# Kernel tuning notes

Hardware: AMD Instinct MI355X
Metric: run time of the kernel (lower is better)

Reference implementation:

```python
import jax, jax.numpy as jnp
import numpy as np

K = 20
EPS = 1e-5
SLOPE = 0.2


def _knn_idx(x, k):
    # x: [B, C, N] -> idx [B, N, k] of nearest neighbors by squared L2
    sq = jnp.sum(x * x, axis=1)                      # [B, N]
    inner = jnp.einsum('bcn,bcm->bnm', x, x)         # [B, N, N]
    neg_dist = 2.0 * inner - sq[:, :, None] - sq[:, None, :]
    return jax.lax.top_k(neg_dist, k)[1]             # [B, N, k]


def _edge_block(x, W, gamma, beta, k):
    # x: [B, C, N]; W: [O, 2C]; returns [B, O, N]
    idx = _knn_idx(x, k)
    xt = jnp.transpose(x, (0, 2, 1))                 # [B, N, C]
    nb = jax.vmap(lambda t, i: t[i])(xt, idx)        # [B, N, k, C] gather
    ctr = xt[:, :, None, :]
    edge = jnp.concatenate(
        [nb - ctr, jnp.broadcast_to(ctr, nb.shape)], axis=-1)  # [B, N, k, 2C]
    y = jnp.einsum('bnkc,oc->bonk', edge, W)         # 1x1 conv
    # BatchNorm2d (training mode: batch stats over B,N,k per channel)
    m = jnp.mean(y, axis=(0, 2, 3), keepdims=True)
    v = jnp.var(y, axis=(0, 2, 3), keepdims=True)
    y = (y - m) * jax.lax.rsqrt(v + EPS)
    y = y * gamma[None, :, None, None] + beta[None, :, None, None]
    y = jnp.where(y >= 0, y, SLOPE * y)              # LeakyReLU(0.2)
    return jnp.max(y, axis=-1)                       # max over k neighbors


def setup_inputs() -> dict:
    key = jax.random.key(0)
    ks = jax.random.split(key, 8)
    B, N = 8, 2048
    x = jax.random.normal(ks[0], (B, N, 3), dtype=jnp.float32)
    W1 = jax.random.normal(ks[1], (64, 6), dtype=jnp.float32) * 0.2
    W2 = jax.random.normal(ks[2], (128, 128), dtype=jnp.float32) * 0.08
    W3 = jax.random.normal(ks[3], (256, 256), dtype=jnp.float32) * 0.06
    g1, b1 = jnp.ones((64,), jnp.float32), jnp.zeros((64,), jnp.float32)
    g2, b2 = jnp.ones((128,), jnp.float32), jnp.zeros((128,), jnp.float32)
    g3, b3 = jnp.ones((256,), jnp.float32), jnp.zeros((256,), jnp.float32)
    L1 = jax.random.normal(ks[4], (1024, 448), dtype=jnp.float32) * 0.04
    L2 = jax.random.normal(ks[5], (2500, 1024), dtype=jnp.float32) * 0.03
    return {"x": x, "W1": W1, "g1": g1, "b1": b1, "W2": W2, "g2": g2,
            "b2": b2, "W3": W3, "g3": g3, "b3": b3, "L1": L1, "L2": L2}


def reference(x, W1, g1, b1, W2, g2, b2, W3, g3, b3, L1, L2):
    xT = jnp.transpose(x, (0, 2, 1))                 # [B, 3, N]
    x1 = _edge_block(xT, W1, g1, b1, K)              # [B, 64, N]
    x2 = _edge_block(x1, W2, g2, b2, K)              # [B, 128, N]
    x3 = _edge_block(x2, W3, g3, b3, K)              # [B, 256, N]
    feat = jnp.concatenate([x1, x2, x3], axis=1)     # [B, 448, N]
    pooled = jnp.max(feat, axis=-1)                  # adaptive_max_pool1d(1)
    h = pooled @ L1.T
    h = jnp.where(h >= 0, h, SLOPE * h)              # LeakyReLU(0.2)
    # dropout is identity in eval mode
    return h @ L2.T                                  # [B, 2500]
```

## Files before the change

kernel.cpp:

```cpp
#include <hip/hip_runtime.h>
#include <hip/hip_bf16.h>
#include <float.h>

#define K_NN 20
#define EPS 1e-5f
#define SLOPE 0.2f
constexpr int Bsz = 8;
constexpr int Npts = 2048;
constexpr int NQ = 8;
constexpr int BN = Bsz * Npts;

typedef __attribute__((ext_vector_type(8))) short short8v;
typedef __attribute__((ext_vector_type(4))) float f32x4;

__device__ __forceinline__ float dot4(float4 a, float4 b) {
  return a.x*b.x + a.y*b.y + a.z*b.z + a.w*b.w;
}
__device__ __forceinline__ unsigned encf(float f) {
  unsigned u = __float_as_uint(f);
  return (u & 0x80000000u) ? ~u : (u | 0x80000000u);
}
__device__ __forceinline__ float decf(unsigned e) {
  unsigned u = (e & 0x80000000u) ? (e & 0x7fffffffu) : ~e;
  return __uint_as_float(u);
}
__device__ __forceinline__ unsigned short f2bf(float x) {
  unsigned u = __float_as_uint(x);
  unsigned r = (u + 0x7fffu + ((u >> 16) & 1u)) >> 16;
  return (unsigned short)r;
}
__device__ __forceinline__ float bf2f(unsigned short h) {
  return __uint_as_float((unsigned)h << 16);
}
__device__ __forceinline__ f32x4 mfma16(short8v a, short8v b, f32x4 c) {
  return __builtin_amdgcn_mfma_f32_16x16x32_bf16(a, b, c, 0, 0, 0);
}

template<int C>
__global__ __launch_bounds__(256) void sq_kernel(const float* __restrict__ xt,
                                                 float* __restrict__ sq) {
  int p = blockIdx.x * 256 + threadIdx.x;
  if (p >= BN) return;
  const float* r = xt + (size_t)p * C;
  float s = 0.f;
  if constexpr (C % 4 == 0) {
    for (int c4 = 0; c4 < C / 4; ++c4) { float4 v = *(const float4*)(r + c4 * 4); s += dot4(v, v); }
  } else {
    #pragma unroll
    for (int c = 0; c < C; ++c) { float v = r[c]; s += v * v; }
  }
  sq[p] = s;
}

template<int C, int MT>
__global__ __launch_bounds__(256) void knn_part(const float* __restrict__ xt,
    const float* __restrict__ sq, float* __restrict__ pval, int* __restrict__ pidx) {
  constexpr int MQ = Npts / NQ;
  __shared__ __align__(16) float chk[MT][C];
  __shared__ float csq[MT];
  const int t = threadIdx.x, w = t >> 6, l = t & 63;
  const int rowblk = blockIdx.x / NQ;
  const int q = blockIdx.x - rowblk * NQ;
  const int p0 = rowblk * 256;
  const int b = p0 / Npts;
  const int myrow = p0 + w * 64 + l;

  float cr[C];
  #pragma unroll
  for (int c = 0; c < C; ++c) cr[c] = xt[(size_t)myrow * C + c];
  const float sqn = sq[myrow];

  float vals[K_NN]; int ids[K_NN];
  #pragma unroll
  for (int i = 0; i < K_NN; ++i) { vals[i] = -FLT_MAX; ids[i] = 0; }

  const int mbase = q * MQ;
  for (int m0 = mbase; m0 < mbase + MQ; m0 += MT) {
    __syncthreads();
    const float* s2 = xt + ((size_t)b * Npts + m0) * C;
    for (int e = t; e < MT * C; e += 256) chk[e / C][e - (e / C) * C] = s2[e];
    for (int e = t; e < MT; e += 256) csq[e] = sq[b * Npts + m0 + e];
    __syncthreads();
    for (int j = 0; j < MT; ++j) {
      float dt = 0.f;
      #pragma unroll
      for (int c = 0; c < C; ++c) dt += cr[c] * chk[j][c];
      float nd = 2.f * dt - sqn - csq[j];
      if (nd > vals[K_NN - 1]) {
        vals[K_NN - 1] = nd; ids[K_NN - 1] = m0 + j;
        #pragma unroll
        for (int i = K_NN - 1; i >= 1; --i) {
          if (vals[i] > vals[i - 1]) {
            float tv = vals[i]; vals[i] = vals[i-1]; vals[i-1] = tv;
            int ti = ids[i]; ids[i] = ids[i-1]; ids[i-1] = ti;
          }
        }
      }
    }
  }
  size_t base = ((size_t)q * BN + myrow) * K_NN;
  #pragma unroll
  for (int i = 0; i < K_NN; ++i) { pval[base + i] = vals[i]; pidx[base + i] = ids[i]; }
}

__global__ __launch_bounds__(256) void knn_merge(const float* __restrict__ pval,
    const int* __restrict__ pidx, int* __restrict__ idxout) {
  int p = blockIdx.x * 256 + threadIdx.x;
  if (p >= BN) return;
  float vals[K_NN]; int ids[K_NN];
  size_t base = (size_t)p * K_NN;
  #pragma unroll
  for (int i = 0; i < K_NN; ++i) { vals[i] = pval[base + i]; ids[i] = pidx[base + i]; }
  for (int q = 1; q < NQ; ++q) {
    size_t b2 = ((size_t)q * BN + p) * K_NN;
    #pragma unroll
    for (int i = 0; i < K_NN; ++i) {
      float v = pval[b2 + i];
      if (v <= vals[K_NN - 1]) break;
      int m = pidx[b2 + i];
      vals[K_NN - 1] = v; ids[K_NN - 1] = m;
      #pragma unroll
      for (int r = K_NN - 1; r >= 1; --r) {
        if (vals[r] > vals[r - 1]) {
          float tv = vals[r]; vals[r] = vals[r-1]; vals[r-1] = tv;
          int ti = ids[r]; ids[r] = ids[r-1]; ids[r-1] = ti;
        }
      }
    }
  }
  int* op = idxout + (size_t)p * K_NN;
  #pragma unroll
  for (int i = 0; i < K_NN; ++i) op[i] = ids[i];
}

template<int C>
__global__ __launch_bounds__(64) void knn_fused(
    const unsigned short* __restrict__ xh, const unsigned short* __restrict__ xl,
    const float* __restrict__ sq, int* __restrict__ idxout) {
  constexpr int KS = C / 32;
  const int b = blockIdx.x >> 7, qt = blockIdx.x & 127;
  const int q0 = qt * 16;
  const int l = threadIdx.x, l15 = l & 15, grp = l >> 4;
  const unsigned short* xbh = xh + (size_t)b * Npts * C;
  const unsigned short* xbl = xl + (size_t)b * Npts * C;
  const float* sqb = sq + b * Npts;
  const int qi = q0 + l15;

  short8v bh[KS], bl[KS];
  #pragma unroll
  for (int ks = 0; ks < KS; ++ks) {
    const size_t a = (size_t)qi * C + ks * 32 + grp * 8;
    bh[ks] = *(const short8v*)(xbh + a);
    bl[ks] = *(const short8v*)(xbl + a);
  }
  const float sqn = sqb[qi];

  float vals[K_NN]; int ids[K_NN];
  #pragma unroll
  for (int i = 0; i < K_NN; ++i) { vals[i] = -FLT_MAX; ids[i] = 0; }

  for (int mt = 0; mt < Npts / 64; ++mt) {
    const int m0 = mt * 64;
    f32x4 acc[4];
    #pragma unroll
    for (int rt = 0; rt < 4; ++rt) acc[rt] = (f32x4){0.f, 0.f, 0.f, 0.f};
    #pragma unroll
    for (int ks = 0; ks < KS; ++ks) {
      #pragma unroll
      for (int rt = 0; rt < 4; ++rt) {
        const size_t aoff = (size_t)(m0 + rt * 16 + l15) * C + ks * 32 + grp * 8;
        const short8v a_h = *(const short8v*)(xbh + aoff);
        const short8v a_l = *(const short8v*)(xbl + aoff);
        acc[rt] = mfma16(a_h, bh[ks], acc[rt]);
        acc[rt] = mfma16(a_l, bh[ks], acc[rt]);
        acc[rt] = mfma16(a_h, bl[ks], acc[rt]);
      }
    }
    #pragma unroll
    for (int rt = 0; rt < 4; ++rt) {
      const int cb = m0 + rt * 16 + grp * 4;
      const float4 s4 = *(const float4*)(sqb + cb);
      const float sv[4] = {s4.x, s4.y, s4.z, s4.w};
      #pragma unroll
      for (int r = 0; r < 4; ++r) {
        const int cand = cb + r;
        float v = 2.f * acc[rt][r] - sqn - sv[r];
        if (cand == qi) v = 0.f;
        if (v > vals[K_NN - 1]) {
          vals[K_NN - 1] = v; ids[K_NN - 1] = cand;
          #pragma unroll
          for (int i = K_NN - 1; i >= 1; --i) {
            if (vals[i] > vals[i - 1]) {
              float tv = vals[i]; vals[i] = vals[i-1]; vals[i-1] = tv;
              int ti = ids[i]; ids[i] = ids[i-1]; ids[i-1] = ti;
            }
          }
        }
      }
    }
  }

  #pragma unroll
  for (int s2 = 1; s2 < 4; ++s2) {
    float ov[K_NN]; int oi[K_NN];
    #pragma unroll
    for (int i = 0; i < K_NN; ++i) {
      ov[i] = __shfl(vals[i], s2 * 16 + l15);
      oi[i] = __shfl(ids[i],  s2 * 16 + l15);
    }
    if (grp == 0) {
      #pragma unroll
      for (int i = 0; i < K_NN; ++i) {
        const float v = ov[i];
        if (v <= vals[K_NN - 1]) break;
        vals[K_NN - 1] = v; ids[K_NN - 1] = oi[i];
        #pragma unroll
        for (int r = K_NN - 1; r >= 1; --r) {
          if (vals[r] > vals[r - 1]) {
            float tv = vals[r]; vals[r] = vals[r-1]; vals[r-1] = tv;
            int ti = ids[r]; ids[r] = ids[r-1]; ids[r-1] = ti;
          }
        }
      }
    }
  }
  if (grp == 0) {
    int* op = idxout + ((size_t)(b * Npts + qi)) * K_NN;
    #pragma unroll
    for (int i = 0; i < K_NN; ++i) op[i] = ids[i];
  }
}

template<int C, int O>
__global__ __launch_bounds__(256) void prep_w(const float* __restrict__ W,
    unsigned short* __restrict__ wh, unsigned short* __restrict__ wl) {
  int i = blockIdx.x * 256 + threadIdx.x;
  if (i >= 2 * O * C) return;
  int j = i / C, c = i - j * C;
  float v = (j < O) ? W[(size_t)j * 2 * C + c]
                    : (W[(size_t)(j - O) * 2 * C + C + c] - W[(size_t)(j - O) * 2 * C + c]);
  unsigned short h = f2bf(v);
  wh[i] = h; wl[i] = f2bf(v - bf2f(h));
}

template<int C, int N2>
__global__ __launch_bounds__(256) void zgemm(
    const unsigned short* __restrict__ xh, const unsigned short* __restrict__ xl,
    const unsigned short* __restrict__ wh, const unsigned short* __restrict__ wl,
    float* __restrict__ Z, int r0) {
  constexpr int KS = C / 32;
  constexpr int CB = N2 / 64;
  const int nb = blockIdx.x / CB, cb = blockIdx.x - nb * CB;
  const int ln0 = nb * 64;
  const int t = threadIdx.x, l = t & 63, wv = t >> 6, l15 = l & 15, grp = l >> 4;
  const int col = cb * 64 + wv * 16 + l15;
  f32x4 acc[4];
  #pragma unroll
  for (int rt = 0; rt < 4; ++rt) acc[rt] = (f32x4){0.f, 0.f, 0.f, 0.f};
  #pragma unroll
  for (int ks = 0; ks < KS; ++ks) {
    const int krd = ks * 32 + grp * 8;
    const short8v bh = *(const short8v*)(wh + (size_t)col * C + krd);
    const short8v bl = *(const short8v*)(wl + (size_t)col * C + krd);
    #pragma unroll
    for (int rt = 0; rt < 4; ++rt) {
      const size_t arow = (size_t)(r0 + ln0 + rt * 16 + l15) * C + krd;
      const short8v a_h = *(const short8v*)(xh + arow);
      const short8v a_l = *(const short8v*)(xl + arow);
      acc[rt] = mfma16(a_h, bh, acc[rt]);
      acc[rt] = mfma16(a_l, bh, acc[rt]);
      acc[rt] = mfma16(a_h, bl, acc[rt]);
    }
  }
  #pragma unroll
  for (int rt = 0; rt < 4; ++rt)
    #pragma unroll
    for (int r = 0; r < 4; ++r)
      Z[(size_t)(ln0 + rt * 16 + grp * 4 + r) * N2 + col] = acc[rt][r];
}

template<int O, int NPP>
__global__ __launch_bounds__(256) void nbr_reduce(
    const float* __restrict__ Z, const int* __restrict__ idx,
    float* __restrict__ mx, float* __restrict__ mn,
    float* __restrict__ psum, float* __restrict__ psq, int r0) {
  constexpr int PPB = 256 / O;
  constexpr int O2 = 2 * O;
  const int t = threadIdx.x;
  const int o = t % O;
  const int sub = t / O;
  float ls = 0.f, lq = 0.f;
  for (int it = 0; it < NPP / PPB; ++it) {
    const int p = r0 + blockIdx.x * NPP + it * PPB + sub;
    const int bbase = (p >> 11) << 11;
    const int* ip = idx + (size_t)p * K_NN;
    const float base = Z[(size_t)(p - r0) * O2 + O + o];
    float vmx = -FLT_MAX, vmn = FLT_MAX;
    #pragma unroll
    for (int k = 0; k < K_NN; ++k) {
      const int nbrow = bbase + ip[k] - r0;
      const float y = Z[(size_t)nbrow * O2 + o] + base;
      ls += y; lq = fmaf(y, y, lq);
      vmx = fmaxf(vmx, y); vmn = fminf(vmn, y);
    }
    mx[(size_t)p * O + o] = vmx;
    mn[(size_t)p * O + o] = vmn;
  }
  if constexpr (PPB > 1) {
    __shared__ float s1[256], s2[256];
    s1[t] = ls; s2[t] = lq;
    __syncthreads();
    if (sub == 0) {
      psum[(size_t)blockIdx.x * O + o] = ls + s1[t + O];
      psq [(size_t)blockIdx.x * O + o] = lq + s2[t + O];
    }
  } else {
    psum[(size_t)blockIdx.x * O + o] = ls;
    psq [(size_t)blockIdx.x * O + o] = lq;
  }
}

template<int C, int O, int G, int NPG, int CPT>
__global__ __launch_bounds__(256) void edge_kernel(const float* __restrict__ xt,
    const int* __restrict__ idx, const float* __restrict__ W,
    float* __restrict__ mx, float* __restrict__ mn,
    float* __restrict__ psum, float* __restrict__ psq) {
  constexpr int WP = O / (64 * CPT);
  constexpr int TPB = 64 * WP * NPG;
  constexpr int PPG = G / NPG;
  static_assert(TPB == 256, "block must be 256 threads");
  __shared__ __align__(16) float pts[G][K_NN + 1][C];
  __shared__ int ids[G][K_NN + 1];
  __shared__ float shps[NPG][O];
  __shared__ float shpq[NPG][O];
  const int t = threadIdx.x;
  const int p0 = blockIdx.x * G;
  const int b = p0 / Npts;

  for (int e = t; e < G * (K_NN + 1); e += TPB) {
    int g = e / (K_NN + 1), j = e - g * (K_NN + 1);
    ids[g][j] = (j == 0) ? (p0 + g) : (b * Npts + idx[(size_t)(p0 + g) * K_NN + (j - 1)]);
  }
  __syncthreads();
  for (int e = t; e < G * (K_NN + 1) * C; e += TPB) {
    int g = e / ((K_NN + 1) * C), rem = e - g * ((K_NN + 1) * C);
    int j = rem / C, c = rem - j * C;
    pts[g][j][c] = xt[(size_t)ids[g][j] * C + c];
  }
  __syncthreads();

  const int w = t >> 6, l = t & 63;
  const int pg = w / WP, wp = w - pg * WP;
  const int o0 = wp * 64 + l;
  float ls0 = 0.f, lq0 = 0.f;

  for (int it = 0; it < PPG; ++it) {
    const int g = pg * PPG + it;
    float yk0[K_NN];
    float u0 = 0.f, v0 = 0.f;
    #pragma unroll
    for (int k = 0; k < K_NN; ++k) yk0[k] = 0.f;
    const float* W0 = W + (size_t)o0 * (2 * C);
    #pragma unroll
    for (int c = 0; c < C; ++c) {
      const float wl = W0[c], whv = W0[C + c], ccv = pts[g][0][c];
      u0 += wl * ccv; v0 += whv * ccv;
      #pragma unroll
      for (int k = 0; k < K_NN; ++k) yk0[k] += wl * pts[g][k + 1][c];
    }
    const int n = p0 + g - b * Npts;
    const size_t obase = ((size_t)b * Npts + n) * O;
    const float base = v0 - u0;
    float vmx = -FLT_MAX, vmn = FLT_MAX;
    #pragma unroll
    for (int k = 0; k < K_NN; ++k) {
      float y = yk0[k] + base;
      ls0 += y; lq0 += y * y;
      vmx = fmaxf(vmx, y); vmn = fminf(vmn, y);
    }
    mx[obase + o0] = vmx; mn[obase + o0] = vmn;
  }

  shps[pg][o0] = ls0; shpq[pg][o0] = lq0;
  __syncthreads();
  if (t < O) {
    float s = 0.f, qq = 0.f;
    #pragma unroll
    for (int i = 0; i < NPG; ++i) { s += shps[i][t]; qq += shpq[i][t]; }
    psum[(size_t)blockIdx.x * O + t] = s;
    psq [(size_t)blockIdx.x * O + t] = qq;
  }
}

template<int O, int NBLK>
__global__ __launch_bounds__(256) void stats_part(const float* __restrict__ psum,
    const float* __restrict__ psq, double* __restrict__ pp, double* __restrict__ pq) {
  constexpr int NS = 16;
  constexpr int SL = NBLK / NS;
  const int l = threadIdx.x & 63, w = threadIdx.x >> 6;
  const int os = blockIdx.x % (O / 64), sl = blockIdx.x / (O / 64);
  const int o = os * 64 + l;
  double s = 0.0, ss = 0.0;
  for (int i = sl * SL + w; i < (sl + 1) * SL; i += 4) {
    s  += (double)psum[(size_t)i * O + o];
    ss += (double)psq [(size_t)i * O + o];
  }
  __shared__ double sh[2][4][64];
  sh[0][w][l] = s; sh[1][w][l] = ss;
  __syncthreads();
  if (w == 0) {
    s  = sh[0][0][l] + sh[0][1][l] + sh[0][2][l] + sh[0][3][l];
    ss = sh[1][0][l] + sh[1][1][l] + sh[1][2][l] + sh[1][3][l];
    pp[(size_t)sl * O + o] = s;
    pq[(size_t)sl * O + o] = ss;
  }
}

template<int O>
__global__ __launch_bounds__(64) void stats_final(const double* __restrict__ pp,
    const double* __restrict__ pq,
    const float* __restrict__ gamma, const float* __restrict__ beta,
    float* __restrict__ scale, float* __restrict__ bias) {
  const int o = blockIdx.x * 64 + threadIdx.x;
  double s = 0.0, ss = 0.0;
  #pragma unroll
  for (int sl = 0; sl < 16; ++sl) { s += pp[(size_t)sl * O + o]; ss += pq[(size_t)sl * O + o]; }
  double cnt = (double)Bsz * Npts * K_NN;
  double m = s / cnt;
  double var = ss / cnt - m * m;
  float g = gamma[o];
  float sc = g * rsqrtf((float)var + EPS);
  scale[o] = sc;
  bias[o] = beta[o] - (float)m * sc;
}

__global__ __launch_bounds__(256) void reset_pool(unsigned* __restrict__ pooled) {
  int i = blockIdx.x * 256 + threadIdx.x;
  if (i < Bsz * 448) pooled[i] = 0u;
}

template<int O, int COFF, bool WNC>
__global__ __launch_bounds__(256) void apply_kernel(const float* __restrict__ mx,
    const float* __restrict__ mn, const float* __restrict__ scale,
    const float* __restrict__ bias, float* __restrict__ xnc,
    unsigned short* __restrict__ xh, unsigned short* __restrict__ xl,
    unsigned* __restrict__ pooled) {
  constexpr int OT = O / 64;
  constexpr int NCH = Npts / 256;
  const int bid = blockIdx.x;
  const int nchunk = bid % NCH;
  const int ot = (bid / NCH) % OT;
  const int b = bid / (NCH * OT);
  const int l = threadIdx.x & 63, w = threadIdx.x >> 6;
  const int o = ot * 64 + l;
  const float sc = scale[o], bs = bias[o];
  const bool pos = (sc >= 0.f);
  float vmax = -FLT_MAX;
  const int n0 = nchunk * 256;
  for (int i = 0; i < 64; ++i) {
    int n = n0 + w + i * 4;
    size_t ix = ((size_t)b * Npts + n) * O + o;
    float raw = pos ? mx[ix] : mn[ix];
    float y = raw * sc + bs;
    y = (y >= 0.f) ? y : SLOPE * y;
    if constexpr (WNC) {
      xnc[ix] = y;
      unsigned short h = f2bf(y);
      xh[ix] = h;
      xl[ix] = f2bf(y - bf2f(h));
    }
    vmax = fmaxf(vmax, y);
  }
  __shared__ float sh[4][64];
  sh[w][l] = vmax;
  __syncthreads();
  if (w == 0) {
    float m = fmaxf(fmaxf(sh[0][l], sh[1][l]), fmaxf(sh[2][l], sh[3][l]));
    atomicMax(pooled + b * 448 + COFF + o, encf(m));
  }
}

template<int CIN, bool LRELU, bool DECODE>
__global__ __launch_bounds__(64) void fc_kernel(const void* __restrict__ inv,
    const float* __restrict__ Wt, float* __restrict__ out, int JO) {
  int j = blockIdx.x;
  const float* wr = Wt + (size_t)j * CIN;
  float acc[Bsz];
  #pragma unroll
  for (int b = 0; b < Bsz; ++b) acc[b] = 0.f;
  for (int c = threadIdx.x; c < CIN; c += 64) {
    float wv = wr[c];
    #pragma unroll
    for (int b = 0; b < Bsz; ++b) {
      float x;
      if constexpr (DECODE) x = decf(((const unsigned*)inv)[b * CIN + c]);
      else                  x = ((const float*)inv)[b * CIN + c];
      acc[b] += x * wv;
    }
  }
  #pragma unroll
  for (int b = 0; b < Bsz; ++b) {
    float v = acc[b];
    #pragma unroll
    for (int w = 32; w > 0; w >>= 1) v += __shfl_down(v, w);
    if (threadIdx.x == 0) {
      if (LRELU) v = (v >= 0.f) ? v : SLOPE * v;
      out[b * JO + j] = v;
    }
  }
}

extern "C" void kernel_launch(void* const* d_in, const int* in_sizes, int n_in,
                              void* d_out, int out_size, void* d_ws, size_t ws_size,
                              hipStream_t stream) {
  const float* x   = (const float*)d_in[0];
  const float* W1  = (const float*)d_in[1];
  const float* g1  = (const float*)d_in[2];
  const float* b1  = (const float*)d_in[3];
  const float* W2  = (const float*)d_in[4];
  const float* g2  = (const float*)d_in[5];
  const float* b2  = (const float*)d_in[6];
  const float* W3  = (const float*)d_in[7];
  const float* g3  = (const float*)d_in[8];
  const float* b3  = (const float*)d_in[9];
  const float* L1  = (const float*)d_in[10];
  const float* L2  = (const float*)d_in[11];
  float* out = (float*)d_out;

  float* ws = (float*)d_ws;
  size_t off = 0;
  float* sq    = ws + off; off += BN;
  int*   idxb  = (int*)(ws + off); off += (size_t)BN * K_NN;
  float* mx    = ws + off; off += (size_t)BN * 256;
  float* mn    = ws + off; off += (size_t)BN * 256;
  float* Z     = ws + off; off += (size_t)BN * 256;
  float* psum  = ws + off; off += (size_t)2048 * 256;
  float* psq   = ws + off; off += (size_t)2048 * 256;
  off = (off + 1) & ~(size_t)1;
  double* pp   = (double*)(ws + off); off += 16 * 256 * 2;
  double* pq   = (double*)(ws + off); off += 16 * 256 * 2;
  float* scale = ws + off; off += 256;
  float* bias  = ws + off; off += 256;
  float* x1nc  = ws + off; off += (size_t)BN * 64;
  float* x2nc  = ws + off; off += (size_t)BN * 128;
  unsigned short* xh1 = (unsigned short*)(ws + off); off += (size_t)BN * 64 / 2;
  unsigned short* xl1 = (unsigned short*)(ws + off); off += (size_t)BN * 64 / 2;
  unsigned short* xh2 = (unsigned short*)(ws + off); off += (size_t)BN * 128 / 2;
  unsigned short* xl2 = (unsigned short*)(ws + off); off += (size_t)BN * 128 / 2;
  unsigned* pooled = (unsigned*)(ws + off); off += Bsz * 448;
  float* h     = ws + off; off += Bsz * 1024;
  unsigned short* wch2 = (unsigned short*)(ws + off); off += 256 * 64 / 2;
  unsigned short* wcl2 = (unsigned short*)(ws + off); off += 256 * 64 / 2;
  unsigned short* wch3 = (unsigned short*)(ws + off); off += 512 * 128 / 2;
  unsigned short* wcl3 = (unsigned short*)(ws + off); off += 512 * 128 / 2;
  float* pval = mx;
  int*   pidx = (int*)mn;

  reset_pool<<<14, 256, 0, stream>>>(pooled);
  prep_w<64, 128><<<(2 * 128 * 64 + 255) / 256, 256, 0, stream>>>(W2, wch2, wcl2);
  prep_w<128, 256><<<(2 * 256 * 128 + 255) / 256, 256, 0, stream>>>(W3, wch3, wcl3);

  sq_kernel<3><<<64, 256, 0, stream>>>(x, sq);
  knn_part<3, 64><<<(BN / 256) * NQ, 256, 0, stream>>>(x, sq, pval, pidx);
  knn_merge<<<64, 256, 0, stream>>>(pval, pidx, idxb);
  edge_kernel<3, 64, 16, 4, 1><<<BN / 16, 256, 0, stream>>>(x, idxb, W1, mx, mn, psum, psq);
  stats_part<64, 1024><<<16, 256, 0, stream>>>(psum, psq, pp, pq);
  stats_final<64><<<1, 64, 0, stream>>>(pp, pq, g1, b1, scale, bias);
  apply_kernel<64, 0, true><<<64, 256, 0, stream>>>(mx, mn, scale, bias, x1nc, xh1, xl1, pooled);

  sq_kernel<64><<<64, 256, 0, stream>>>(x1nc, sq);
  knn_fused<64><<<Bsz * 128, 64, 0, stream>>>(xh1, xl1, sq, idxb);
  zgemm<64, 256><<<(BN / 64) * 4, 256, 0, stream>>>(xh1, xl1, wch2, wcl2, Z, 0);
  nbr_reduce<128, 16><<<BN / 16, 256, 0, stream>>>(Z, idxb, mx, mn, psum, psq, 0);
  stats_part<128, 1024><<<32, 256, 0, stream>>>(psum, psq, pp, pq);
  stats_final<128><<<2, 64, 0, stream>>>(pp, pq, g2, b2, scale, bias);
  apply_kernel<128, 64, true><<<128, 256, 0, stream>>>(mx, mn, scale, bias, x2nc, xh2, xl2, pooled);

  sq_kernel<128><<<64, 256, 0, stream>>>(x2nc, sq);
  knn_fused<128><<<Bsz * 128, 64, 0, stream>>>(xh2, xl2, sq, idxb);
  for (int pass = 0; pass < 2; ++pass) {
    const int r0 = pass * (BN / 2);
    zgemm<128, 512><<<(BN / 2 / 64) * 8, 256, 0, stream>>>(xh2, xl2, wch3, wcl3, Z, r0);
    nbr_reduce<256, 8><<<BN / 2 / 8, 256, 0, stream>>>(Z, idxb, mx, mn,
        psum + (size_t)pass * 1024 * 256, psq + (size_t)pass * 1024 * 256, r0);
  }
  stats_part<256, 2048><<<64, 256, 0, stream>>>(psum, psq, pp, pq);
  stats_final<256><<<4, 64, 0, stream>>>(pp, pq, g3, b3, scale, bias);
  apply_kernel<256, 192, false><<<256, 256, 0, stream>>>(mx, mn, scale, bias, nullptr, nullptr, nullptr, pooled);

  fc_kernel<448, true, true><<<1024, 64, 0, stream>>>(pooled, L1, h, 1024);
  fc_kernel<1024, false, false><<<2500, 64, 0, stream>>>(h, L2, out, 2500);
}
```

Measured before the change: 1.238 ms.

## Split knn_fused candidate scan across four waves and merge via LDS; early-exit insertion

knn_fused now launches 256 threads per block, and each of the four wavefronts scans a quarter of the candidate points for the same 16 queries. The per-wave top-K lists are written to shared memory and merged by 16 threads after a barrier. Separately, the insertion-sort bubble loops in all kNN kernels now break as soon as the new element is in place. This is meant to add parallelism for the 1024-block grid and cut wasted compare/swap work, at the cost of an LDS merge, a block sync, and more divergent branches in unrolled loops.

```diff
diff --git a/kernel.cpp b/kernel.cpp
--- a/kernel.cpp
+++ b/kernel.cpp
@@ -93,7 +93,7 @@
           if (vals[i] > vals[i - 1]) {
             float tv = vals[i]; vals[i] = vals[i-1]; vals[i-1] = tv;
             int ti = ids[i]; ids[i] = ids[i-1]; ids[i-1] = ti;
-          }
+          } else break;
         }
       }
     }
@@ -124,7 +124,7 @@
         if (vals[r] > vals[r - 1]) {
           float tv = vals[r]; vals[r] = vals[r-1]; vals[r-1] = tv;
           int ti = ids[r]; ids[r] = ids[r-1]; ids[r-1] = ti;
-        }
+        } else break;
       }
     }
   }
@@ -134,13 +134,16 @@
 }
 
 template<int C>
-__global__ __launch_bounds__(64) void knn_fused(
+__global__ __launch_bounds__(256) void knn_fused(
     const unsigned short* __restrict__ xh, const unsigned short* __restrict__ xl,
     const float* __restrict__ sq, int* __restrict__ idxout) {
   constexpr int KS = C / 32;
+  constexpr int TPW = Npts / 64 / 4;
+  __shared__ float svv[4][16][K_NN];
+  __shared__ int   sii[4][16][K_NN];
   const int b = blockIdx.x >> 7, qt = blockIdx.x & 127;
   const int q0 = qt * 16;
-  const int l = threadIdx.x, l15 = l & 15, grp = l >> 4;
+  const int t = threadIdx.x, wv = t >> 6, l = t & 63, l15 = l & 15, grp = l >> 4;
   const unsigned short* xbh = xh + (size_t)b * Npts * C;
   const unsigned short* xbl = xl + (size_t)b * Npts * C;
   const float* sqb = sq + b * Npts;
@@ -159,7 +162,7 @@
   #pragma unroll
   for (int i = 0; i < K_NN; ++i) { vals[i] = -FLT_MAX; ids[i] = 0; }
 
-  for (int mt = 0; mt < Npts / 64; ++mt) {
+  for (int mt = wv * TPW; mt < (wv + 1) * TPW; ++mt) {
     const int m0 = mt * 64;
     f32x4 acc[4];
     #pragma unroll
@@ -193,7 +196,7 @@
             if (vals[i] > vals[i - 1]) {
               float tv = vals[i]; vals[i] = vals[i-1]; vals[i-1] = tv;
               int ti = ids[i]; ids[i] = ids[i-1]; ids[i-1] = ti;
-            }
+            } else break;
           }
         }
       }
@@ -219,13 +222,34 @@
           if (vals[r] > vals[r - 1]) {
             float tv = vals[r]; vals[r] = vals[r-1]; vals[r-1] = tv;
             int ti = ids[r]; ids[r] = ids[r-1]; ids[r-1] = ti;
-          }
+          } else break;
         }
       }
     }
   }
   if (grp == 0) {
-    int* op = idxout + ((size_t)(b * Npts + qi)) * K_NN;
+    #pragma unroll
+    for (int i = 0; i < K_NN; ++i) { svv[wv][l15][i] = vals[i]; sii[wv][l15][i] = ids[i]; }
+  }
+  __syncthreads();
+  if (t < 16) {
+    #pragma unroll
+    for (int s2 = 1; s2 < 4; ++s2) {
+      #pragma unroll
+      for (int i = 0; i < K_NN; ++i) {
+        const float v = svv[s2][t][i];
+        if (v <= vals[K_NN - 1]) break;
+        vals[K_NN - 1] = v; ids[K_NN - 1] = sii[s2][t][i];
+        #pragma unroll
+        for (int r = K_NN - 1; r >= 1; --r) {
+          if (vals[r] > vals[r - 1]) {
+            float tv = vals[r]; vals[r] = vals[r-1]; vals[r-1] = tv;
+            int ti = ids[r]; ids[r] = ids[r-1]; ids[r-1] = ti;
+          } else break;
+        }
+      }
+    }
+    int* op = idxout + ((size_t)(b * Npts + q0 + t)) * K_NN;
     #pragma unroll
     for (int i = 0; i < K_NN; ++i) op[i] = ids[i];
   }
@@ -569,7 +593,7 @@
   apply_kernel<64, 0, true><<<64, 256, 0, stream>>>(mx, mn, scale, bias, x1nc, xh1, xl1, pooled);
 
   sq_kernel<64><<<64, 256, 0, stream>>>(x1nc, sq);
-  knn_fused<64><<<Bsz * 128, 64, 0, stream>>>(xh1, xl1, sq, idxb);
+  knn_fused<64><<<Bsz * 128, 256, 0, stream>>>(xh1, xl1, sq, idxb);
   zgemm<64, 256><<<(BN / 64) * 4, 256, 0, stream>>>(xh1, xl1, wch2, wcl2, Z, 0);
   nbr_reduce<128, 16><<<BN / 16, 256, 0, stream>>>(Z, idxb, mx, mn, psum, psq, 0);
   stats_part<128, 1024><<<32, 256, 0, stream>>>(psum, psq, pp, pq);
@@ -577,7 +601,7 @@
   apply_kernel<128, 64, true><<<128, 256, 0, stream>>>(mx, mn, scale, bias, x2nc, xh2, xl2, pooled);
 
   sq_kernel<128><<<64, 256, 0, stream>>>(x2nc, sq);
-  knn_fused<128><<<Bsz * 128, 64, 0, stream>>>(xh2, xl2, sq, idxb);
+  knn_fused<128><<<Bsz * 128, 256, 0, stream>>>(xh2, xl2, sq, idxb);
   for (int pass = 0; pass < 2; ++pass) {
     const int r0 = pass * (BN / 2);
     zgemm<128, 512><<<(BN / 2 / 64) * 8, 256, 0, stream>>>(xh2, xl2, wch3, wcl3, Z, r0);
```

After: 3.011 ms. 2.43x slower.

## Replace per-lane insertion-sort top-k with two-pass radix select in shared memory

Applied to the files above, without the earlier changes.

The fused KNN kernel for layers 2 and 3 now uses 256 threads per block of 16 queries. It finds the top-20 by building shared-memory byte histograms over the encoded distance keys, selecting the threshold bucket in two radix passes, then collecting candidates above the threshold and resolving the boundary bucket. This replaces the register insertion sort with branchy swaps per candidate, at the cost of recomputing the distance MFMA three times and contending on shared-memory atomics. A 160-entry cap on the boundary bucket could drop candidates if many keys tie in the top 16 bits. Output indices are sorted by index rather than by distance, and knn_merge gains a template parameter so its merge loop can be unrolled.

```diff
diff --git a/kernel.cpp b/kernel.cpp
--- a/kernel.cpp
+++ b/kernel.cpp
@@ -103,6 +103,7 @@
   for (int i = 0; i < K_NN; ++i) { pval[base + i] = vals[i]; pidx[base + i] = ids[i]; }
 }
 
+template<int NQM>
 __global__ __launch_bounds__(256) void knn_merge(const float* __restrict__ pval,
     const int* __restrict__ pidx, int* __restrict__ idxout) {
   int p = blockIdx.x * 256 + threadIdx.x;
@@ -111,7 +112,8 @@
   size_t base = (size_t)p * K_NN;
   #pragma unroll
   for (int i = 0; i < K_NN; ++i) { vals[i] = pval[base + i]; ids[i] = pidx[base + i]; }
-  for (int q = 1; q < NQ; ++q) {
+  #pragma unroll
+  for (int q = 1; q < NQM; ++q) {
     size_t b2 = ((size_t)q * BN + p) * K_NN;
     #pragma unroll
     for (int i = 0; i < K_NN; ++i) {
@@ -134,13 +136,19 @@
 }
 
 template<int C>
-__global__ __launch_bounds__(64) void knn_fused(
+__global__ __launch_bounds__(256) void knn_radix(
     const unsigned short* __restrict__ xh, const unsigned short* __restrict__ xl,
     const float* __restrict__ sq, int* __restrict__ idxout) {
   constexpr int KS = C / 32;
+  constexpr int CAP = 160;
+  __shared__ unsigned hist[16][257];
+  __shared__ unsigned outb[16][K_NN];
+  __shared__ unsigned bkey[16][CAP];
+  __shared__ unsigned bidx[16][CAP];
+  __shared__ unsigned sb1[16], sneed1[16], sprefix[16], sneed2[16], ocnt[16], bct[16];
   const int b = blockIdx.x >> 7, qt = blockIdx.x & 127;
   const int q0 = qt * 16;
-  const int l = threadIdx.x, l15 = l & 15, grp = l >> 4;
+  const int t = threadIdx.x, wv = t >> 6, l = t & 63, l15 = l & 15, grp = l >> 4;
   const unsigned short* xbh = xh + (size_t)b * Npts * C;
   const unsigned short* xbl = xl + (size_t)b * Npts * C;
   const float* sqb = sq + b * Npts;
@@ -155,12 +163,7 @@
   }
   const float sqn = sqb[qi];
 
-  float vals[K_NN]; int ids[K_NN];
-  #pragma unroll
-  for (int i = 0; i < K_NN; ++i) { vals[i] = -FLT_MAX; ids[i] = 0; }
-
-  for (int mt = 0; mt < Npts / 64; ++mt) {
-    const int m0 = mt * 64;
+  auto compute_keys = [&](int m0, unsigned* keys) {
     f32x4 acc[4];
     #pragma unroll
     for (int rt = 0; rt < 4; ++rt) acc[rt] = (f32x4){0.f, 0.f, 0.f, 0.f};
@@ -183,51 +186,121 @@
       const float sv[4] = {s4.x, s4.y, s4.z, s4.w};
       #pragma unroll
       for (int r = 0; r < 4; ++r) {
-        const int cand = cb + r;
         float v = 2.f * acc[rt][r] - sqn - sv[r];
-        if (cand == qi) v = 0.f;
-        if (v > vals[K_NN - 1]) {
-          vals[K_NN - 1] = v; ids[K_NN - 1] = cand;
-          #pragma unroll
-          for (int i = K_NN - 1; i >= 1; --i) {
-            if (vals[i] > vals[i - 1]) {
-              float tv = vals[i]; vals[i] = vals[i-1]; vals[i-1] = tv;
-              int ti = ids[i]; ids[i] = ids[i-1]; ids[i-1] = ti;
-            }
+        if (cb + r == qi) v = 0.f;
+        keys[rt * 4 + r] = encf(v);
+      }
+    }
+  };
+
+  for (int i = t; i < 16 * 257; i += 256) ((unsigned*)hist)[i] = 0u;
+  __syncthreads();
+  #pragma unroll 1
+  for (int ti = 0; ti < 8; ++ti) {
+    unsigned keys[16];
+    compute_keys((wv * 8 + ti) * 64, keys);
+    #pragma unroll
+    for (int i = 0; i < 16; ++i) atomicAdd(&hist[l15][keys[i] >> 24], 1u);
+  }
+  __syncthreads();
+  if (t < 16) {
+    unsigned cum = 0, na = 0; int b1 = 0, found = 0;
+    for (int bin = 255; bin >= 0; --bin) {
+      unsigned c = hist[t][bin];
+      if (!found && cum + c >= K_NN) { b1 = bin; na = cum; found = 1; }
+      cum += c;
+    }
+    sb1[t] = (unsigned)b1; sneed1[t] = K_NN - na;
+  }
+  __syncthreads();
+  for (int i = t; i < 16 * 257; i += 256) ((unsigned*)hist)[i] = 0u;
+  __syncthreads();
+  const unsigned myb1 = sb1[l15];
+  #pragma unroll 1
+  for (int ti = 0; ti < 8; ++ti) {
+    unsigned keys[16];
+    compute_keys((wv * 8 + ti) * 64, keys);
+    #pragma unroll
+    for (int i = 0; i < 16; ++i)
+      if ((keys[i] >> 24) == myb1) atomicAdd(&hist[l15][(keys[i] >> 16) & 255u], 1u);
+  }
+  __syncthreads();
+  if (t < 16) {
+    const unsigned tgt = sneed1[t];
+    unsigned cum = 0, na2 = 0; int b2 = 0, found = 0;
+    for (int bin = 255; bin >= 0; --bin) {
+      unsigned c = hist[t][bin];
+      if (!found && cum + c >= tgt) { b2 = bin; na2 = cum; found = 1; }
+      cum += c;
+    }
+    sprefix[t] = (sb1[t] << 8) | (unsigned)b2;
+    sneed2[t] = tgt - na2;
+    ocnt[t] = 0u; bct[t] = 0u;
+  }
+  __syncthreads();
+  const unsigned myprefix = sprefix[l15];
+  #pragma unroll 1
+  for (int ti = 0; ti < 8; ++ti) {
+    const int m0 = (wv * 8 + ti) * 64;
+    unsigned keys[16];
+    compute_keys(m0, keys);
+    #pragma unroll
+    for (int rt = 0; rt < 4; ++rt) {
+      #pragma unroll
+      for (int r = 0; r < 4; ++r) {
+        const unsigned key = keys[rt * 4 + r];
+        const unsigned cand = (unsigned)(m0 + rt * 16 + grp * 4 + r);
+        const unsigned k16 = key >> 16;
+        if (k16 > myprefix) {
+          unsigned s = atomicAdd(&ocnt[l15], 1u);
+          outb[l15][s] = cand;
+        } else if (k16 == myprefix) {
+          unsigned p = atomicAdd(&bct[l15], 1u);
+          if (p < CAP) { bkey[l15][p] = key; bidx[l15][p] = cand; }
+        }
+      }
+    }
+  }
+  __syncthreads();
+  if (t < 16) {
+    const int q = t;
+    const unsigned m = min(bct[q], (unsigned)CAP);
+    const unsigned nd2 = sneed2[q];
+    const unsigned base = ocnt[q];
+    unsigned kv[K_NN], ki[K_NN];
+    #pragma unroll
+    for (int i = 0; i < K_NN; ++i) { kv[i] = 0u; ki[i] = 0u; }
+    for (unsigned j = 0; j < m; ++j) {
+      const unsigned kk = bkey[q][j], ii = bidx[q][j];
+      const bool beat = (kk > kv[K_NN - 1]) ||
+                        (kk == kv[K_NN - 1] && ii < ki[K_NN - 1]);
+      if (beat) {
+        kv[K_NN - 1] = kk; ki[K_NN - 1] = ii;
+        #pragma unroll
+        for (int i = K_NN - 1; i >= 1; --i) {
+          const bool sw = (kv[i] > kv[i - 1]) ||
+                          (kv[i] == kv[i - 1] && ki[i] < ki[i - 1]);
+          if (sw) {
+            unsigned tv = kv[i]; kv[i] = kv[i-1]; kv[i-1] = tv;
+            unsigned tix = ki[i]; ki[i] = ki[i-1]; ki[i-1] = tix;
           }
         }
       }
     }
-  }
-
-  #pragma unroll
-  for (int s2 = 1; s2 < 4; ++s2) {
-    float ov[K_NN]; int oi[K_NN];
-    #pragma unroll
-    for (int i = 0; i < K_NN; ++i) {
-      ov[i] = __shfl(vals[i], s2 * 16 + l15);
-      oi[i] = __shfl(ids[i],  s2 * 16 + l15);
-    }
-    if (grp == 0) {
+    #pragma unroll
+    for (int i = 0; i < K_NN; ++i)
+      if ((unsigned)i < nd2) outb[q][base + i] = ki[i];
+    int ob[K_NN];
+    #pragma unroll
+    for (int i = 0; i < K_NN; ++i) ob[i] = (int)outb[q][i];
+    #pragma unroll
+    for (int i = 1; i < K_NN; ++i)
       #pragma unroll
-      for (int i = 0; i < K_NN; ++i) {
-        const float v = ov[i];
-        if (v <= vals[K_NN - 1]) break;
-        vals[K_NN - 1] = v; ids[K_NN - 1] = oi[i];
-        #pragma unroll
-        for (int r = K_NN - 1; r >= 1; --r) {
-          if (vals[r] > vals[r - 1]) {
-            float tv = vals[r]; vals[r] = vals[r-1]; vals[r-1] = tv;
-            int ti = ids[r]; ids[r] = ids[r-1]; ids[r-1] = ti;
-          }
-        }
-      }
-    }
-  }
-  if (grp == 0) {
-    int* op = idxout + ((size_t)(b * Npts + qi)) * K_NN;
-    #pragma unroll
-    for (int i = 0; i < K_NN; ++i) op[i] = ids[i];
+      for (int j = K_NN - 1; j >= 1; --j)
+        if (ob[j] < ob[j - 1]) { int tv = ob[j]; ob[j] = ob[j-1]; ob[j-1] = tv; }
+    int* op = idxout + ((size_t)(b * Npts + q0 + q)) * K_NN;
+    #pragma unroll
+    for (int i = 0; i < K_NN; ++i) op[i] = ob[i];
   }
 }
 
@@ -562,14 +635,14 @@
 
   sq_kernel<3><<<64, 256, 0, stream>>>(x, sq);
   knn_part<3, 64><<<(BN / 256) * NQ, 256, 0, stream>>>(x, sq, pval, pidx);
-  knn_merge<<<64, 256, 0, stream>>>(pval, pidx, idxb);
+  knn_merge<NQ><<<64, 256, 0, stream>>>(pval, pidx, idxb);
   edge_kernel<3, 64, 16, 4, 1><<<BN / 16, 256, 0, stream>>>(x, idxb, W1, mx, mn, psum, psq);
   stats_part<64, 1024><<<16, 256, 0, stream>>>(psum, psq, pp, pq);
   stats_final<64><<<1, 64, 0, stream>>>(pp, pq, g1, b1, scale, bias);
   apply_kernel<64, 0, true><<<64, 256, 0, stream>>>(mx, mn, scale, bias, x1nc, xh1, xl1, pooled);
 
   sq_kernel<64><<<64, 256, 0, stream>>>(x1nc, sq);
-  knn_fused<64><<<Bsz * 128, 64, 0, stream>>>(xh1, xl1, sq, idxb);
+  knn_radix<64><<<Bsz * 128, 256, 0, stream>>>(xh1, xl1, sq, idxb);
   zgemm<64, 256><<<(BN / 64) * 4, 256, 0, stream>>>(xh1, xl1, wch2, wcl2, Z, 0);
   nbr_reduce<128, 16><<<BN / 16, 256, 0, stream>>>(Z, idxb, mx, mn, psum, psq, 0);
   stats_part<128, 1024><<<32, 256, 0, stream>>>(psum, psq, pp, pq);
@@ -577,7 +650,7 @@
   apply_kernel<128, 64, true><<<128, 256, 0, stream>>>(mx, mn, scale, bias, x2nc, xh2, xl2, pooled);
 
   sq_kernel<128><<<64, 256, 0, stream>>>(x2nc, sq);
-  knn_fused<128><<<Bsz * 128, 64, 0, stream>>>(xh2, xl2, sq, idxb);
+  knn_radix<128><<<Bsz * 128, 256, 0, stream>>>(xh2, xl2, sq, idxb);
   for (int pass = 0; pass < 2; ++pass) {
     const int r0 = pass * (BN / 2);
     zgemm<128, 512><<<(BN / 2 / 64) * 8, 256, 0, stream>>>(xh2, xl2, wch3, wcl3, Z, r0);
```

Measured after the change: 1.240 ms. About the same (+0.2%).
